# Kernel optimization log

Hardware: AMD Instinct MI355X
Metric: run time of the kernel (lower is better)

## Reference

```python
import jax, jax.numpy as jnp
import numpy as np


def setup_inputs() -> dict:
    key = jax.random.key(0)
    ks = jax.random.split(key, 12)
    N, T, V, C, O, IC, S = 32, 256, 25, 64, 64, 16, 3
    rn = lambda k, sh, s=1.0: jax.random.normal(k, sh, dtype=jnp.float32) * s
    return {
        "x": rn(ks[0], (N, T, V, C)),
        "A": jax.random.uniform(ks[1], (S, V, V), dtype=jnp.float32),
        "PA": rn(ks[2], (S, V, V), 0.01),
        "weight_A": jax.random.uniform(ks[3], (4,), dtype=jnp.float32),
        "Wa": rn(ks[4], (S, C, IC), 1.0 / np.sqrt(C)),
        "ba": rn(ks[5], (S, IC), 0.01),
        "Wb": rn(ks[6], (S, C, IC), 1.0 / np.sqrt(C)),
        "bb": rn(ks[7], (S, IC), 0.01),
        "Wd": rn(ks[8], (S, C, O), 1.0 / np.sqrt(C)),
        "bd": rn(ks[9], (S, O), 0.01),
        "gamma": jax.random.uniform(ks[10], (O,), dtype=jnp.float32),
        "beta": rn(ks[11], (O,), 0.1),
    }


def reference(x, A, PA, weight_A, Wa, ba, Wb, bb, Wd, bd, gamma, beta):
    # unit_gcn_confirm forward (in_channels == out_channels, so `down` = identity)
    N, T, V, C = x.shape
    S, _, IC = Wa.shape
    BN_EPS = 1e-5

    # A = w0 * A_static + w1 * softmax(PA)  -> (S, V, V)
    A_comb = weight_A[0] * A + weight_A[1] * jax.nn.softmax(PA, axis=-1)

    # per-subset Q/K projections: (S, N, T, V, IC)
    qa = jnp.einsum('ntvc,sci->sntvi', x, Wa) + ba[:, None, None, None, :]
    kb = jnp.einsum('ntvc,sci->sntvi', x, Wb) + bb[:, None, None, None, :]

    # A1: time-flattened attention over nodes, scale sqrt(IC*T) -> (S, N, V, V)
    A1 = jax.nn.softmax(
        jnp.einsum('sntui,sntvi->snuv', qa, kb) / jnp.sqrt(jnp.float32(IC * T)),
        axis=-1)
    # A2: per-frame attention over nodes, scale sqrt(IC) -> (S, N, T, V, V)
    A2 = jax.nn.softmax(
        jnp.einsum('sntui,sntvi->sntuv', qa, kb) / jnp.sqrt(jnp.float32(IC)),
        axis=-1)

    # combined adjacency per subset: (S, N, T, V, V)
    A_in = (A_comb[:, None, None, :, :]
            + weight_A[2] * A1[:, :, None, :, :]
            + weight_A[3] * A2)

    # message passing + per-subset output linear, summed over subsets
    z = jnp.einsum('sntuv,ntvc->sntuc', A_in, x)             # (S, N, T, V, C)
    y = jnp.einsum('sntuc,sco->ntuo', z, Wd) + bd.sum(0)     # (N, T, V, O)

    # BatchNorm2d in inference mode (running_mean=0, running_var=1)
    y = y * (gamma / jnp.sqrt(1.0 + BN_EPS)) + beta

    # residual (down = identity since in_channels == out_channels) + relu
    return jax.nn.relu(y + x)
```

## Files before the change

### kernel.cpp

```cpp
#include <hip/hip_runtime.h>
#include <hip/hip_bf16.h>

typedef __hip_bfloat16 bf16;
typedef __attribute__((ext_vector_type(8))) short short8;
typedef __attribute__((ext_vector_type(4))) float f32x4;

#define S  3
#define V  25
#define C  64
#define O  64
#define IC 16
#define NN 32
#define TT 256
#define TB 2
#define TCH 8

__device__ __forceinline__ float b2f(bf16 v) { return __bfloat162float(v); }

__device__ __forceinline__ float ldv(const void* p, size_t i, int f32) {
    return f32 ? ((const float*)p)[i] : b2f(((const bf16*)p)[i]);
}

__device__ __forceinline__ unsigned short f2bf(float f) {
    bf16 h = __float2bfloat16(f);
    return *(unsigned short*)&h;
}

__global__ __launch_bounds__(256) void k_prep(
    const void* __restrict__ x,
    const void* __restrict__ A, const void* __restrict__ PA,
    const void* __restrict__ wA,
    const void* __restrict__ Wa, const void* __restrict__ Wb,
    const void* __restrict__ Wd,
    float* __restrict__ A_comb, float* __restrict__ S1,
    unsigned short* __restrict__ wprep, int* __restrict__ flagp) {
    __shared__ int sflag;
    if (threadIdx.x < 64) {
        const bf16* p = (const bf16*)x;
        int bad = 0;
        #pragma unroll
        for (int k = 0; k < 32; k++) {
            float v = b2f(p[threadIdx.x + k * 64]);
            bad |= !(v > -1000.f && v < 1000.f);
        }
        unsigned long long m = __ballot(bad);
        if (threadIdx.x == 0) {
            sflag = (m != 0ull) ? 1 : 0;
            if (blockIdx.x == 0) *flagp = sflag;
        }
    }
    __syncthreads();
    int f32 = sflag;

    int g = blockIdx.x * 256 + threadIdx.x;
    int stride = gridDim.x * 256;

    for (int w = g; w < 60000; w += stride) S1[w] = 0.f;

    for (int w = g; w < 3456; w += stride) {
        int s = w / 1152, r = w % 1152, i = r / 72, c = r % 72;
        unsigned short va = 0, vb = 0;
        if (c < 64) {
            va = f2bf(ldv(Wa, (size_t)s * 1024 + c * 16 + i, f32));
            vb = f2bf(ldv(Wb, (size_t)s * 1024 + c * 16 + i, f32));
        }
        wprep[s * 6912 + i * 72 + c] = va;
        wprep[s * 6912 + 1152 + i * 72 + c] = vb;
    }
    for (int w = g; w < 13824; w += stride) {
        int s = w / 4608, r = w % 4608, o = r / 72, c = r % 72;
        unsigned short vd = 0;
        if (c < 64) vd = f2bf(ldv(Wd, (size_t)s * 4096 + c * 64 + o, f32));
        wprep[s * 6912 + 2304 + o * 72 + c] = vd;
    }

    if (g < S * V) {
        float w0 = ldv(wA, 0, f32), w1 = ldv(wA, 1, f32);
        float vals[V];
        float m = -1e30f;
        for (int v = 0; v < V; v++) { vals[v] = ldv(PA, g * V + v, f32); m = fmaxf(m, vals[v]); }
        float sum = 0.f;
        for (int v = 0; v < V; v++) { vals[v] = __expf(vals[v] - m); sum += vals[v]; }
        float inv = 1.f / sum;
        for (int v = 0; v < V; v++)
            A_comb[g * V + v] = w0 * ldv(A, g * V + v, f32) + w1 * vals[v] * inv;
    }
}

#define P1_QK(sidx, QB, KB) do {                                              \
    const unsigned short* wat_ = wqk + (sidx) * 2304;                         \
    short8 wa0 = *(const short8*)&wat_[lm * 72 + kq * 8];                     \
    short8 wa1 = *(const short8*)&wat_[lm * 72 + 32 + kq * 8];                \
    short8 wb0 = *(const short8*)&wat_[1152 + lm * 72 + kq * 8];              \
    short8 wb1 = *(const short8*)&wat_[1152 + lm * 72 + 32 + kq * 8];         \
    f32x4 q = __builtin_amdgcn_mfma_f32_16x16x32_bf16(xa0, wa0, (f32x4){0.f,0.f,0.f,0.f}, 0, 0, 0); \
    q = __builtin_amdgcn_mfma_f32_16x16x32_bf16(xa1, wa1, q, 0, 0, 0);        \
    f32x4 k = __builtin_amdgcn_mfma_f32_16x16x32_bf16(xa0, wb0, (f32x4){0.f,0.f,0.f,0.f}, 0, 0, 0); \
    k = __builtin_amdgcn_mfma_f32_16x16x32_bf16(xa1, wb1, k, 0, 0, 0);        \
    _Pragma("unroll")                                                         \
    for (int reg = 0; reg < 4; reg++) {                                       \
        (QB)[(drow0 + reg) * 20 + lm] = f2bf(q[reg] + rbq[sidx]);             \
        (KB)[(drow0 + reg) * 20 + lm] = f2bf(k[reg] + rbk[sidx]);             \
    }                                                                         \
} while (0)

#define E_ACC(AC, QB, KB) do {                                                \
    short8 a_ = *(const short8*)&(QB)[(tsel + ur0 + lm) * 20 + ksel];         \
    short8 b_ = *(const short8*)&(KB)[(tsel + vc0 + lm) * 20 + ksel];         \
    (AC) = __builtin_amdgcn_mfma_f32_16x16x32_bf16(a_, b_, (AC), 0, 0, 0);    \
} while (0)

#define STAGE_XB(TTOFF) do {                                                  \
    if (f32) {                                                                \
        const float4* xp = (const float4*)x + (size_t)(n * TT + t0 + (TTOFF)) * 400; \
        for (int w = tid; w < 800; w += 256) {                                \
            int t = w / 400, r = w % 400, u = r >> 4, c4 = r & 15;            \
            float4 v = xp[w];                                                 \
            unsigned short h[4] = {f2bf(v.x), f2bf(v.y), f2bf(v.z), f2bf(v.w)}; \
            *(uint2*)&xb[(t * 32 + u) * 72 + c4 * 4] = *(uint2*)h;            \
        }                                                                     \
    } else {                                                                  \
        const unsigned int* xp = (const unsigned int*)x;                      \
        size_t base2 = (size_t)(n * TT + t0 + (TTOFF)) * V * C / 2;           \
        for (int w = tid; w < 1600; w += 256) {                               \
            int t = w / 800, r = w % 800, u = r >> 5, c2 = r & 31;            \
            ((unsigned int*)xb)[(t * 32 + u) * 36 + c2] = xp[base2 + (size_t)(t * V + u) * 32 + c2]; \
        }                                                                     \
    }                                                                         \
} while (0)

__global__ __launch_bounds__(256) void k_s1(
    const void* __restrict__ x,
    const unsigned short* __restrict__ wprep,
    const void* __restrict__ ba, const void* __restrict__ bb,
    float* __restrict__ S1g, const int* __restrict__ flagp) {
    int f32 = *flagp;
    int tchunk = blockIdx.x, n = blockIdx.y;
    int tid = threadIdx.x;
    int lane = tid & 63, wv = tid >> 6;
    int lm = lane & 15, kq = lane >> 4;

    __shared__ __align__(16) unsigned short xb[64 * 72];
    __shared__ __align__(16) unsigned short wqk[3 * 2304];
    __shared__ __align__(16) unsigned short qab0[64 * 20];
    __shared__ __align__(16) unsigned short qab1[64 * 20];
    __shared__ __align__(16) unsigned short kbb0[64 * 20];
    __shared__ __align__(16) unsigned short kbb1[64 * 20];

    for (int w = tid; w < 864; w += 256) {
        int s = w / 288, off = w % 288;
        ((uint4*)wqk)[w] = ((const uint4*)(wprep + (size_t)s * 6912))[off];
    }
    float rbq[3], rbk[3];
    #pragma unroll
    for (int s = 0; s < 3; s++) {
        rbq[s] = ldv(ba, s * IC + lm, f32);
        rbk[s] = ldv(bb, s * IC + lm, f32);
    }

    int mrow = wv * 16 + lm;
    int drow0 = wv * 16 + (kq << 2);
    int ur0 = ((wv >> 1) & 1) << 4;
    int vc0 = (wv & 1) << 4;
    int t0 = tchunk * TCH;
    int tsel = (kq >> 1) << 5;
    int ksel = (kq & 1) << 3;

    f32x4 acc0 = {0.f,0.f,0.f,0.f}, acc1 = {0.f,0.f,0.f,0.f}, acc2 = {0.f,0.f,0.f,0.f};

    STAGE_XB(0);
    __syncthreads();

    for (int pp = 0; pp < TCH / 2; pp++) {
        short8 xa0 = *(const short8*)&xb[mrow * 72 + kq * 8];
        short8 xa1 = *(const short8*)&xb[mrow * 72 + 32 + kq * 8];
        P1_QK(0, qab0, kbb0);
        __syncthreads();
        E_ACC(acc0, qab0, kbb0);
        P1_QK(1, qab1, kbb1);
        __syncthreads();
        E_ACC(acc1, qab1, kbb1);
        P1_QK(2, qab0, kbb0);
        __syncthreads();
        E_ACC(acc2, qab0, kbb0);
        if (pp < TCH / 2 - 1) STAGE_XB(2 * pp + 2);
        __syncthreads();
    }

    {
        int u = ur0 + (kq << 2), v = vc0 + lm;
        float* d0 = S1g + (size_t)n * 625;
        float* d1 = S1g + ((size_t)NN + n) * 625;
        float* d2 = S1g + ((size_t)2 * NN + n) * 625;
        #pragma unroll
        for (int reg = 0; reg < 4; reg++) {
            if (u + reg < V && v < V) {
                atomicAdd(&d0[(u + reg) * 25 + v], acc0[reg]);
                atomicAdd(&d1[(u + reg) * 25 + v], acc1[reg]);
                atomicAdd(&d2[(u + reg) * 25 + v], acc2[reg]);
            }
        }
    }
}

__global__ void k_a1(float* __restrict__ S1g, const float* __restrict__ A_comb,
                     const void* __restrict__ wA, const int* __restrict__ flagp) {
    int f32 = *flagp;
    float w2 = ldv(wA, 2, f32);
    int sn = blockIdx.x;
    int s = sn / NN;
    int u = threadIdx.x;
    if (u >= V) return;
    float* row = S1g + (size_t)sn * V * V + u * V;
    const float* ac = A_comb + (size_t)(s * V + u) * V;
    const float scale = 1.0f / 64.0f;
    float vals[V];
    float m = -1e30f;
    for (int v = 0; v < V; v++) { vals[v] = row[v] * scale; m = fmaxf(m, vals[v]); }
    float sum = 0.f;
    for (int v = 0; v < V; v++) { vals[v] = __expf(vals[v] - m); sum += vals[v]; }
    float inv = w2 / sum;
    for (int v = 0; v < V; v++) row[v] = ac[v] + vals[v] * inv;
}

__global__ __launch_bounds__(256, 5) void k_main(
    const void* __restrict__ x,
    const void* __restrict__ ba, const void* __restrict__ bb,
    const void* __restrict__ bd,
    const void* __restrict__ gamma, const void* __restrict__ beta,
    const void* __restrict__ wA,
    const unsigned short* __restrict__ wprep,
    const float* __restrict__ ac1g,
    void* __restrict__ outp, const int* __restrict__ flagp) {
    int f32 = *flagp;
    int bx = blockIdx.x;
    int n = bx >> 7, tc = bx & 127;
    int t0 = tc * TB;
    int tid = threadIdx.x;
    int lane = tid & 63, wv = tid >> 6;
    int lm = lane & 15, kq = lane >> 4;

    __shared__ __align__(16) unsigned short xb[64 * 72];
    __shared__ __align__(16) unsigned short qab[64 * 40];
    __shared__ __align__(16) unsigned short kbb[64 * 40];
    __shared__ __align__(16) unsigned short xwtb[2 * 64 * 40];
    __shared__ float gs[O], bts[O], bds[O];

    if (f32) {
        const float4* xp = (const float4*)x + (size_t)(n * TT + t0) * 400;
        for (int w = tid; w < 800; w += 256) {
            int t = w / 400, r = w % 400, u = r >> 4, c4 = r & 15;
            float4 v = xp[w];
            unsigned short h[4] = {f2bf(v.x), f2bf(v.y), f2bf(v.z), f2bf(v.w)};
            *(uint2*)&xb[(t * 32 + u) * 72 + c4 * 4] = *(uint2*)h;
        }
    } else {
        const unsigned int* xp = (const unsigned int*)x;
        size_t base2 = (size_t)(n * TT + t0) * V * C / 2;
        for (int w = tid; w < 1600; w += 256) {
            int t = w / 800, r = w % 800, u = r >> 5, c2 = r & 31;
            ((unsigned int*)xb)[(t * 32 + u) * 36 + c2] = xp[base2 + (size_t)(t * V + u) * 32 + c2];
        }
    }
    for (int w = tid; w < 14 * 36; w += 256) {
        int idx = w / 36, word = w % 36;
        int row = (idx < 7) ? (25 + idx) : (32 + 25 + idx - 7);
        ((unsigned int*)xb)[row * 36 + word] = 0;
    }
    for (int w = tid; w < 50 * 4; w += 256) {
        int idx = w >> 2, word = 32 + (w & 3);
        int row = (idx < 25) ? idx : (32 + idx - 25);
        ((unsigned int*)xb)[row * 36 + word] = 0;
    }
    for (int w = tid; w < 512; w += 256) {
        int r = w >> 3, cw = 8 + (w & 7);
        ((unsigned int*)qab)[r * 20 + cw] = 0;
        ((unsigned int*)kbb)[r * 20 + cw] = 0;
    }
    if (tid < O) {
        bds[tid] = ldv(bd, tid, f32) + ldv(bd, O + tid, f32) + ldv(bd, 2 * O + tid, f32);
        gs[tid] = ldv(gamma, tid, f32) * rsqrtf(1.f + 1e-5f);
        bts[tid] = ldv(beta, tid, f32);
    }
    float w3 = ldv(wA, 3, f32);

    f32x4 acc[4];
    #pragma unroll
    for (int nt = 0; nt < 4; nt++) acc[nt] = (f32x4){0.f, 0.f, 0.f, 0.f};

    int t_ = wv >> 1;
    int mrow = wv * 16 + lm;
    int drow0 = wv * 16 + (kq << 2);
    int ub = ((wv & 1) << 4) + (kq << 2);

    __syncthreads();

    short8 xa0 = *(const short8*)&xb[mrow * 72 + kq * 8];
    short8 xa1 = *(const short8*)&xb[mrow * 72 + 32 + kq * 8];

    for (int s = 0; s < S; s++) {
        const unsigned short* watg = wprep + s * 6912;
        const unsigned short* wbtg = watg + 1152;
        const unsigned short* wdtg = watg + 2304;
        const float* acn = ac1g + ((size_t)s * NN + n) * 625;

        {
            short8 wa0 = *(const short8*)&watg[lm * 72 + kq * 8];
            short8 wa1 = *(const short8*)&watg[lm * 72 + 32 + kq * 8];
            short8 wb0 = *(const short8*)&wbtg[lm * 72 + kq * 8];
            short8 wb1 = *(const short8*)&wbtg[lm * 72 + 32 + kq * 8];
            float bq_c = ldv(ba, s * IC + lm, f32);
            float bk_c = ldv(bb, s * IC + lm, f32);
            f32x4 q = __builtin_amdgcn_mfma_f32_16x16x32_bf16(xa0, wa0, (f32x4){0.f,0.f,0.f,0.f}, 0, 0, 0);
            q = __builtin_amdgcn_mfma_f32_16x16x32_bf16(xa1, wa1, q, 0, 0, 0);
            f32x4 k = __builtin_amdgcn_mfma_f32_16x16x32_bf16(xa0, wb0, (f32x4){0.f,0.f,0.f,0.f}, 0, 0, 0);
            k = __builtin_amdgcn_mfma_f32_16x16x32_bf16(xa1, wb1, k, 0, 0, 0);
            #pragma unroll
            for (int reg = 0; reg < 4; reg++) {
                qab[(drow0 + reg) * 40 + lm] = f2bf(q[reg] + bq_c);
                kbb[(drow0 + reg) * 40 + lm] = f2bf(k[reg] + bk_c);
            }
        }
        {
            #pragma unroll
            for (int nt = 0; nt < 4; nt++) {
                short8 wd0 = *(const short8*)&wdtg[(nt * 16 + lm) * 72 + kq * 8];
                short8 wd1 = *(const short8*)&wdtg[(nt * 16 + lm) * 72 + 32 + kq * 8];
                f32x4 xw = __builtin_amdgcn_mfma_f32_16x16x32_bf16(xa0, wd0, (f32x4){0.f,0.f,0.f,0.f}, 0, 0, 0);
                xw = __builtin_amdgcn_mfma_f32_16x16x32_bf16(xa1, wd1, xw, 0, 0, 0);
                unsigned short h[4] = {f2bf(xw[0]), f2bf(xw[1]), f2bf(xw[2]), f2bf(xw[3])};
                *(uint2*)&xwtb[t_ * 2560 + (nt * 16 + lm) * 40 + ub] = *(uint2*)h;
            }
        }
        __syncthreads();

        {
            short8 aq = *(const short8*)&qab[mrow * 40 + kq * 8];
            short8 bk0 = *(const short8*)&kbb[(t_ * 32 + lm) * 40 + kq * 8];
            short8 bk1 = *(const short8*)&kbb[(t_ * 32 + 16 + lm) * 40 + kq * 8];
            f32x4 e0 = __builtin_amdgcn_mfma_f32_16x16x32_bf16(aq, bk0, (f32x4){0.f,0.f,0.f,0.f}, 0, 0, 0);
            f32x4 e1 = __builtin_amdgcn_mfma_f32_16x16x32_bf16(aq, bk1, (f32x4){0.f,0.f,0.f,0.f}, 0, 0, 0);
            #pragma unroll
            for (int reg = 0; reg < 4; reg++) {
                float p0 = __expf(e0[reg] * 0.25f);
                float p1 = (lm < V - 16) ? __expf(e1[reg] * 0.25f) : 0.f;
                float pr = p0 + p1;
                pr += __shfl_xor(pr, 1);
                pr += __shfl_xor(pr, 2);
                pr += __shfl_xor(pr, 4);
                pr += __shfl_xor(pr, 8);
                float si = w3 / pr;
                int u = ub + reg;
                int uc = (u < V) ? u : 0;
                float a0v = (u < V) ? (acn[uc * 25 + lm] + si * p0) : 0.f;
                float a1v = (u < V && lm < V - 16) ? (acn[uc * 25 + 16 + lm] + si * p1) : 0.f;
                qab[(drow0 + reg) * 40 + lm] = f2bf(a0v);
                qab[(drow0 + reg) * 40 + 16 + lm] = f2bf(a1v);
            }
        }
        {
            short8 aA = *(const short8*)&qab[mrow * 40 + kq * 8];
            #pragma unroll
            for (int nt = 0; nt < 4; nt++) {
                short8 bx8 = *(const short8*)&xwtb[t_ * 2560 + (nt * 16 + lm) * 40 + kq * 8];
                acc[nt] = __builtin_amdgcn_mfma_f32_16x16x32_bf16(aA, bx8, acc[nt], 0, 0, 0);
            }
            if (s < S - 1) {
                #pragma unroll
                for (int reg = 0; reg < 4; reg++)
                    qab[(drow0 + reg) * 40 + 16 + lm] = 0;
            }
        }
        __syncthreads();
    }

    if (f32) {
        #pragma unroll
        for (int nt = 0; nt < 4; nt++) {
            int o = nt * 16 + lm;
            float g = gs[o], bt_ = bts[o], bsum = bds[o];
            #pragma unroll
            for (int reg = 0; reg < 4; reg++) {
                int grow = drow0 + reg;
                int t = grow >> 5, u = grow & 31;
                if (u < V) {
                    float xres = b2f(*(const bf16*)&xb[grow * 72 + o]);
                    float yv = fmaxf((acc[nt][reg] + bsum) * g + bt_ + xres, 0.f);
                    size_t ob = (size_t)((n * TT + t0 + t) * V + u) * O + o;
                    ((float*)outp)[ob] = yv;
                }
            }
        }
    } else {
        unsigned short* ep = xwtb;
        #pragma unroll
        for (int nt = 0; nt < 4; nt++) {
            int o = nt * 16 + lm;
            float g = gs[o], bt_ = bts[o], bsum = bds[o];
            #pragma unroll
            for (int reg = 0; reg < 4; reg++) {
                int grow = drow0 + reg;
                int t = grow >> 5, u = grow & 31;
                if (u < V) {
                    float xres = b2f(*(const bf16*)&xb[grow * 72 + o]);
                    float yv = fmaxf((acc[nt][reg] + bsum) * g + bt_ + xres, 0.f);
                    ep[(t * V + u) * O + o] = f2bf(yv);
                }
            }
        }
        __syncthreads();
        uint4* outv = (uint4*)((bf16*)outp + (size_t)(n * TT + t0) * V * O);
        const uint4* epv = (const uint4*)ep;
        for (int w = tid; w < 400; w += 256) outv[w] = epv[w];
    }
}

extern "C" void kernel_launch(void* const* d_in, const int* in_sizes, int n_in,
                              void* d_out, int out_size, void* d_ws, size_t ws_size,
                              hipStream_t stream) {
    const void* x     = d_in[0];
    const void* A     = d_in[1];
    const void* PA    = d_in[2];
    const void* wA    = d_in[3];
    const void* Wa    = d_in[4];
    const void* ba    = d_in[5];
    const void* Wb    = d_in[6];
    const void* bb    = d_in[7];
    const void* Wd    = d_in[8];
    const void* bd    = d_in[9];
    const void* gamma = d_in[10];
    const void* beta  = d_in[11];

    int*   flagp  = (int*)d_ws;
    float* wsf    = (float*)d_ws;
    float* A_comb = wsf + 64;
    float* S1     = wsf + 2048;
    unsigned short* wprep = (unsigned short*)(wsf + 65536);

    k_prep<<<64, 256, 0, stream>>>(x, A, PA, wA, Wa, Wb, Wd, A_comb, S1, wprep, flagp);
    k_s1<<<dim3(TT / TCH, NN), 256, 0, stream>>>(x, wprep, ba, bb, S1, flagp);
    k_a1<<<S * NN, 64, 0, stream>>>(S1, A_comb, wA, flagp);
    k_main<<<NN * TT / TB, 256, 0, stream>>>(x, ba, bb, bd, gamma, beta, wA,
                                             wprep, S1, d_out, flagp);
}
```

Before: 214.0 us.

## Fuse A1 softmax into main kernel and cut syncs in S1 accumulation

Removes the separate k_a1 launch. Each k_main block now recomputes the A1 softmax for its batch element and subset in shared memory, adding the static adjacency before use. k_s1 keeps three Q/K buffers so all three subsets are projected before a single barrier, replacing three barriers per step. The BN and bias constants are now read from global memory directly instead of being staged in shared memory. The trade-off is redundant serial softmax work in every main-kernel block, done by only 25 threads, on that block's critical path.

```diff
diff --git a/kernel.cpp b/kernel.cpp
--- a/kernel.cpp
+++ b/kernel.cpp
@@ -142,10 +142,8 @@
 
     __shared__ __align__(16) unsigned short xb[64 * 72];
     __shared__ __align__(16) unsigned short wqk[3 * 2304];
-    __shared__ __align__(16) unsigned short qab0[64 * 20];
-    __shared__ __align__(16) unsigned short qab1[64 * 20];
-    __shared__ __align__(16) unsigned short kbb0[64 * 20];
-    __shared__ __align__(16) unsigned short kbb1[64 * 20];
+    __shared__ __align__(16) unsigned short qb[3][64 * 20];
+    __shared__ __align__(16) unsigned short kb_[3][64 * 20];
 
     for (int w = tid; w < 864; w += 256) {
         int s = w / 288, off = w % 288;
@@ -174,15 +172,13 @@
     for (int pp = 0; pp < TCH / 2; pp++) {
         short8 xa0 = *(const short8*)&xb[mrow * 72 + kq * 8];
         short8 xa1 = *(const short8*)&xb[mrow * 72 + 32 + kq * 8];
-        P1_QK(0, qab0, kbb0);
+        P1_QK(0, qb[0], kb_[0]);
+        P1_QK(1, qb[1], kb_[1]);
+        P1_QK(2, qb[2], kb_[2]);
         __syncthreads();
-        E_ACC(acc0, qab0, kbb0);
-        P1_QK(1, qab1, kbb1);
-        __syncthreads();
-        E_ACC(acc1, qab1, kbb1);
-        P1_QK(2, qab0, kbb0);
-        __syncthreads();
-        E_ACC(acc2, qab0, kbb0);
+        E_ACC(acc0, qb[0], kb_[0]);
+        E_ACC(acc1, qb[1], kb_[1]);
+        E_ACC(acc2, qb[2], kb_[2]);
         if (pp < TCH / 2 - 1) STAGE_XB(2 * pp + 2);
         __syncthreads();
     }
@@ -201,26 +197,6 @@
             }
         }
     }
-}
-
-__global__ void k_a1(float* __restrict__ S1g, const float* __restrict__ A_comb,
-                     const void* __restrict__ wA, const int* __restrict__ flagp) {
-    int f32 = *flagp;
-    float w2 = ldv(wA, 2, f32);
-    int sn = blockIdx.x;
-    int s = sn / NN;
-    int u = threadIdx.x;
-    if (u >= V) return;
-    float* row = S1g + (size_t)sn * V * V + u * V;
-    const float* ac = A_comb + (size_t)(s * V + u) * V;
-    const float scale = 1.0f / 64.0f;
-    float vals[V];
-    float m = -1e30f;
-    for (int v = 0; v < V; v++) { vals[v] = row[v] * scale; m = fmaxf(m, vals[v]); }
-    float sum = 0.f;
-    for (int v = 0; v < V; v++) { vals[v] = __expf(vals[v] - m); sum += vals[v]; }
-    float inv = w2 / sum;
-    for (int v = 0; v < V; v++) row[v] = ac[v] + vals[v] * inv;
 }
 
 __global__ __launch_bounds__(256, 5) void k_main(
@@ -230,7 +206,8 @@
     const void* __restrict__ gamma, const void* __restrict__ beta,
     const void* __restrict__ wA,
     const unsigned short* __restrict__ wprep,
-    const float* __restrict__ ac1g,
+    const float* __restrict__ S1g,
+    const float* __restrict__ A_comb,
     void* __restrict__ outp, const int* __restrict__ flagp) {
     int f32 = *flagp;
     int bx = blockIdx.x;
@@ -244,7 +221,10 @@
     __shared__ __align__(16) unsigned short qab[64 * 40];
     __shared__ __align__(16) unsigned short kbb[64 * 40];
     __shared__ __align__(16) unsigned short xwtb[2 * 64 * 40];
-    __shared__ float gs[O], bts[O], bds[O];
+    __shared__ __align__(16) float ac1f[640];
+
+    float w2 = ldv(wA, 2, f32);
+    float w3 = ldv(wA, 3, f32);
 
     if (f32) {
         const float4* xp = (const float4*)x + (size_t)(n * TT + t0) * 400;
@@ -277,12 +257,21 @@
         ((unsigned int*)qab)[r * 20 + cw] = 0;
         ((unsigned int*)kbb)[r * 20 + cw] = 0;
     }
-    if (tid < O) {
-        bds[tid] = ldv(bd, tid, f32) + ldv(bd, O + tid, f32) + ldv(bd, 2 * O + tid, f32);
-        gs[tid] = ldv(gamma, tid, f32) * rsqrtf(1.f + 1e-5f);
-        bts[tid] = ldv(beta, tid, f32);
-    }
-    float w3 = ldv(wA, 3, f32);
+    if (tid < V) {
+        int u = tid;
+        const float* row = S1g + (size_t)n * 625 + u * 25;
+        const float* ac = A_comb + (size_t)u * V;
+        float vals[V];
+        float m = -1e30f;
+        #pragma unroll
+        for (int v = 0; v < V; v++) { vals[v] = row[v] * (1.0f / 64.0f); m = fmaxf(m, vals[v]); }
+        float sum = 0.f;
+        #pragma unroll
+        for (int v = 0; v < V; v++) { vals[v] = __expf(vals[v] - m); sum += vals[v]; }
+        float inv = w2 / sum;
+        #pragma unroll
+        for (int v = 0; v < V; v++) ac1f[u * 25 + v] = ac[v] + vals[v] * inv;
+    }
 
     f32x4 acc[4];
     #pragma unroll
@@ -299,10 +288,25 @@
     short8 xa1 = *(const short8*)&xb[mrow * 72 + 32 + kq * 8];
 
     for (int s = 0; s < S; s++) {
+        if (s > 0 && tid < V) {
+            int u = tid;
+            const float* row = S1g + ((size_t)s * NN + n) * 625 + u * 25;
+            const float* ac = A_comb + (size_t)(s * V + u) * V;
+            float vals[V];
+            float m = -1e30f;
+            #pragma unroll
+            for (int v = 0; v < V; v++) { vals[v] = row[v] * (1.0f / 64.0f); m = fmaxf(m, vals[v]); }
+            float sum = 0.f;
+            #pragma unroll
+            for (int v = 0; v < V; v++) { vals[v] = __expf(vals[v] - m); sum += vals[v]; }
+            float inv = w2 / sum;
+            #pragma unroll
+            for (int v = 0; v < V; v++) ac1f[u * 25 + v] = ac[v] + vals[v] * inv;
+        }
+
         const unsigned short* watg = wprep + s * 6912;
         const unsigned short* wbtg = watg + 1152;
         const unsigned short* wdtg = watg + 2304;
-        const float* acn = ac1g + ((size_t)s * NN + n) * 625;
 
         {
             short8 wa0 = *(const short8*)&watg[lm * 72 + kq * 8];
@@ -352,8 +356,8 @@
                 float si = w3 / pr;
                 int u = ub + reg;
                 int uc = (u < V) ? u : 0;
-                float a0v = (u < V) ? (acn[uc * 25 + lm] + si * p0) : 0.f;
-                float a1v = (u < V && lm < V - 16) ? (acn[uc * 25 + 16 + lm] + si * p1) : 0.f;
+                float a0v = (u < V) ? (ac1f[uc * 25 + lm] + si * p0) : 0.f;
+                float a1v = (u < V && lm < V - 16) ? (ac1f[uc * 25 + 16 + lm] + si * p1) : 0.f;
                 qab[(drow0 + reg) * 40 + lm] = f2bf(a0v);
                 qab[(drow0 + reg) * 40 + 16 + lm] = f2bf(a1v);
             }
@@ -378,7 +382,9 @@
         #pragma unroll
         for (int nt = 0; nt < 4; nt++) {
             int o = nt * 16 + lm;
-            float g = gs[o], bt_ = bts[o], bsum = bds[o];
+            float g = ldv(gamma, o, f32) * rsqrtf(1.f + 1e-5f);
+            float bt_ = ldv(beta, o, f32);
+            float bsum = ldv(bd, o, f32) + ldv(bd, O + o, f32) + ldv(bd, 2 * O + o, f32);
             #pragma unroll
             for (int reg = 0; reg < 4; reg++) {
                 int grow = drow0 + reg;
@@ -396,7 +402,9 @@
         #pragma unroll
         for (int nt = 0; nt < 4; nt++) {
             int o = nt * 16 + lm;
-            float g = gs[o], bt_ = bts[o], bsum = bds[o];
+            float g = ldv(gamma, o, f32) * rsqrtf(1.f + 1e-5f);
+            float bt_ = ldv(beta, o, f32);
+            float bsum = ldv(bd, o, f32) + ldv(bd, O + o, f32) + ldv(bd, 2 * O + o, f32);
             #pragma unroll
             for (int reg = 0; reg < 4; reg++) {
                 int grow = drow0 + reg;
@@ -439,7 +447,6 @@
 
     k_prep<<<64, 256, 0, stream>>>(x, A, PA, wA, Wa, Wb, Wd, A_comb, S1, wprep, flagp);
     k_s1<<<dim3(TT / TCH, NN), 256, 0, stream>>>(x, wprep, ba, bb, S1, flagp);
-    k_a1<<<S * NN, 64, 0, stream>>>(S1, A_comb, wA, flagp);
     k_main<<<NN * TT / TB, 256, 0, stream>>>(x, ba, bb, bd, gamma, beta, wA,
-                                             wprep, S1, d_out, flagp);
-}
+                                             wprep, S1, A_comb, d_out, flagp);
+}
```

Result: slower. 257.4 us (+20.2%).
